# Kernel optimization log

Measured on AMD Instinct MI355X. Metric: run time of the kernel, lower is better.

The kernel has to match this reference:

```python
import jax, jax.numpy as jnp
import numpy as np

TEMPERATURE = 0.07
BASE_TEMPERATURE = 0.07


def setup_inputs() -> dict:
    key = jax.random.key(0)
    k1, k2 = jax.random.split(key)
    features = jax.random.normal(k1, (4096, 2, 128), dtype=jnp.float32)
    labels = jax.random.randint(k2, (4096,), 0, 100, dtype=jnp.int64)
    return {"features": features, "labels": labels}


def reference(features, labels):
    # features: [B, n_views, D], labels: [B]
    B, n_views, D = features.shape
    N = B * n_views

    # label equality mask [B, B]
    lab = labels.reshape(-1, 1)
    mask = (lab == lab.T).astype(jnp.float32)

    # flatten views (C-order, same as torch .view) and L2-normalize
    feat = features.reshape(N, D)
    feat = feat / jnp.clip(jnp.linalg.norm(feat, axis=1, keepdims=True), 1e-12)

    # similarity logits [N, N]
    logits = jnp.matmul(feat, feat.T) / TEMPERATURE
    logits_max = jax.lax.stop_gradient(jnp.max(logits, axis=1, keepdims=True))
    logits = logits - logits_max

    # tile mask to [N, N] (torch .repeat ordering) and remove self-contrast
    mask = jnp.tile(mask, (n_views, n_views))
    logits_mask = 1.0 - jnp.eye(N, dtype=jnp.float32)
    mask = mask * logits_mask

    exp_logits = jnp.exp(logits) * logits_mask
    log_prob = logits - jnp.log(jnp.sum(exp_logits, axis=1, keepdims=True) + 1e-12)

    mask_pos_pairs = jnp.clip(jnp.sum(mask, axis=1), 1.0)
    mean_log_prob_pos = jnp.sum(mask * log_prob, axis=1) / mask_pos_pairs

    loss = -(TEMPERATURE / BASE_TEMPERATURE) * mean_log_prob_pos
    return jnp.mean(loss.reshape(n_views, B))
```

## Files before the change

### kernel.cpp

```cpp
#include <hip/hip_runtime.h>
#include <hip/hip_bf16.h>
#include <hip/hip_fp8.h>
#include <math.h>

#define NB 4096
#define NN 8192
#define DD 128
#define NCLS 100
#define NSPLIT 16
#define CHUNK 64
#define NCHUNK 8

constexpr float INV_T = 14.285714285714286f;
constexpr float EC1   = 20.609929155556620f;
constexpr float EC0   = -20.609929155556620f;
constexpr float LN2   = 0.6931471805599453f;

typedef unsigned char u8;
typedef __attribute__((ext_vector_type(8))) int   v8i;
typedef __attribute__((ext_vector_type(4))) int   v4i;
typedef __attribute__((ext_vector_type(4))) float f32x4;

__global__ __launch_bounds__(256) void k_norm(const float* __restrict__ feat,
                                              u8* __restrict__ fb8,
                                              float* __restrict__ selfdot,
                                              float* __restrict__ out) {
    const int gid = blockIdx.x * 256 + threadIdx.x;
    if (gid == 0) out[0] = 0.0f;
    const int r    = gid >> 6;
    const int lane = threadIdx.x & 63;
    const float2 v = ((const float2*)(feat + (size_t)r * DD))[lane];
    float ss = v.x * v.x + v.y * v.y;
#pragma unroll
    for (int off = 1; off < 64; off <<= 1) ss += __shfl_xor(ss, off, 64);
    const float scale = 1.0f / fmaxf(sqrtf(ss), 1e-12f);
    const __hip_fp8_e4m3 qx(v.x * scale), qy(v.y * scale);
    const unsigned short pack = (unsigned short)qx.__x |
                                ((unsigned short)qy.__x << 8);
    ((unsigned short*)(fb8 + (size_t)r * DD))[lane] = pack;
    const float xb = (float)qx, yb = (float)qy;
    float s2 = xb * xb + yb * yb;
#pragma unroll
    for (int off = 1; off < 64; off <<= 1) s2 += __shfl_xor(s2, off, 64);
    if (lane == 0) selfdot[r] = s2;
}

__device__ __forceinline__ void stage_chunk(const u8* __restrict__ fb8, u8* sbuf,
                                            int jb, int w, int n15, int q) {
#pragma unroll
    for (int h = 0; h < 2; ++h) {
        const int p = w * 2 + h;
        const u8* g = fb8 + (size_t)(jb + (p >> 1) * 16 + n15) * DD + q * 32 + (p & 1) * 16;
        __builtin_amdgcn_global_load_lds(
            (const __attribute__((address_space(1))) void*)g,
            (__attribute__((address_space(3))) void*)(sbuf + p * 1024),
            16, 0, 0);
    }
}

__global__ __launch_bounds__(256, 4) void k_main(const u8* __restrict__ fb8,
                                                 const int* __restrict__ labels,
                                                 float* __restrict__ g_se,
                                                 float* __restrict__ g_ps) {
    __shared__ u8 sB[2][CHUNK * DD];
    __shared__ int slab[512];

    const int tid  = threadIdx.x;
    const int lane = tid & 63;
    const int w    = tid >> 6;
    const int rb   = blockIdx.x >> 4;
    const int js   = blockIdx.x & (NSPLIT - 1);
    const int i0   = rb * 128 + w * 32;
    const int jb0  = js * 512;
    const int q    = lane >> 4;
    const int n15  = lane & 15;

    slab[tid]       = labels[(jb0 + tid) & (NB - 1)];
    slab[tid + 256] = labels[(jb0 + tid + 256) & (NB - 1)];

    v8i af[2];
#pragma unroll
    for (int tt = 0; tt < 2; ++tt) {
        const u8* rp = fb8 + (size_t)(i0 + tt * 16 + n15) * DD + q * 32;
        const v4i lo = *(const v4i*)rp;
        const v4i hi = *(const v4i*)(rp + 16);
        v8i a;
#pragma unroll
        for (int k = 0; k < 4; ++k) { a[k] = lo[k]; a[4 + k] = hi[k]; }
        af[tt] = a;
    }
    int labi[8];
#pragma unroll
    for (int tt = 0; tt < 2; ++tt)
#pragma unroll
        for (int r = 0; r < 4; ++r)
            labi[tt * 4 + r] = labels[(i0 + tt * 16 + q * 4 + r) & (NB - 1)];

    float a_se[8] = {}, a_ps[8] = {};

    stage_chunk(fb8, &sB[0][0], jb0, w, n15, q);
    __syncthreads();

    for (int c = 0; c < NCHUNK; ++c) {
        if (c + 1 < NCHUNK)
            stage_chunk(fb8, &sB[(c + 1) & 1][0], jb0 + (c + 1) * CHUNK, w, n15, q);
        const u8* sb = &sB[c & 1][0];
        const int crel = c * CHUNK;
#pragma unroll
        for (int jt = 0; jt < 4; ++jt) {
            const v4i lo = *(const v4i*)(sb + (jt * 2 + 0) * 1024 + lane * 16);
            const v4i hi = *(const v4i*)(sb + (jt * 2 + 1) * 1024 + lane * 16);
            v8i bb;
#pragma unroll
            for (int k = 0; k < 4; ++k) { bb[k] = lo[k]; bb[4 + k] = hi[k]; }
            const int labj = slab[crel + jt * 16 + n15];
            f32x4 a0 = {0.f, 0.f, 0.f, 0.f}, a1 = {0.f, 0.f, 0.f, 0.f};
            a0 = __builtin_amdgcn_mfma_scale_f32_16x16x128_f8f6f4(
                     af[0], bb, a0, 0, 0, 0, 0x7F7F7F7F, 0, 0x7F7F7F7F);
            a1 = __builtin_amdgcn_mfma_scale_f32_16x16x128_f8f6f4(
                     af[1], bb, a1, 0, 0, 0, 0x7F7F7F7F, 0, 0x7F7F7F7F);
#pragma unroll
            for (int r = 0; r < 4; ++r) {
                const float d0 = a0[r], d1 = a1[r];
                a_se[r]     += __builtin_amdgcn_exp2f(fmaf(d0, EC1, EC0));
                a_se[4 + r] += __builtin_amdgcn_exp2f(fmaf(d1, EC1, EC0));
                a_ps[r]     += (labi[r]     == labj) ? d0 : 0.0f;
                a_ps[4 + r] += (labi[4 + r] == labj) ? d1 : 0.0f;
            }
        }
        __syncthreads();
    }

#pragma unroll
    for (int s = 0; s < 8; ++s) {
        float v1 = a_se[s], v2 = a_ps[s];
#pragma unroll
        for (int off = 1; off < 16; off <<= 1) {
            v1 += __shfl_xor(v1, off, 64);
            v2 += __shfl_xor(v2, off, 64);
        }
        if (n15 == 0) {
            const int row = i0 + (s >> 2) * 16 + q * 4 + (s & 3);
            g_se[js * NN + row] = v1;
            g_ps[js * NN + row] = v2;
        }
    }
}

__global__ __launch_bounds__(256) void k_final(const int* __restrict__ labels,
                                               const float* __restrict__ g_se,
                                               const float* __restrict__ g_ps,
                                               const float* __restrict__ selfdot,
                                               float* __restrict__ out) {
    __shared__ int hist[NCLS];
    const int tid = threadIdx.x;
    for (int i = tid; i < NCLS; i += 256) hist[i] = 0;
    __syncthreads();
    for (int b = tid; b < NB; b += 256) atomicAdd(&hist[labels[b]], 1);
    __syncthreads();

    const int r = blockIdx.x * 256 + tid;
    const int c = labels[r & (NB - 1)];
    float se = 0.f, ps = 0.f;
#pragma unroll
    for (int t = 0; t < NSPLIT; ++t) {
        se += g_se[t * NN + r];
        ps += g_ps[t * NN + r];
    }
    const float sd = selfdot[r];
    se -= __builtin_amdgcn_exp2f(fmaf(sd, EC1, EC0));
    const float ct = (float)(2 * hist[c] - 1);
    const float possum = INV_T * ((ps - sd) - ct);
    const float lg  = __builtin_amdgcn_logf(se + 1e-12f) * LN2;
    const float mlpp = (possum - ct * lg) / fmaxf(ct, 1.0f);
    float v = -mlpp * (1.0f / (float)NN);
#pragma unroll
    for (int off = 1; off < 64; off <<= 1) v += __shfl_xor(v, off, 64);
    __shared__ float sred[4];
    if ((tid & 63) == 0) sred[tid >> 6] = v;
    __syncthreads();
    if (tid == 0) atomicAdd(out, sred[0] + sred[1] + sred[2] + sred[3]);
}

extern "C" void kernel_launch(void* const* d_in, const int* in_sizes, int n_in,
                              void* d_out, int out_size, void* d_ws, size_t ws_size,
                              hipStream_t stream) {
    const float* feat = (const float*)d_in[0];
    const int* labels = (const int*)d_in[1];
    float* out        = (float*)d_out;
    char* ws          = (char*)d_ws;

    u8* fb8         = (u8*)ws;
    float* g_se     = (float*)(ws + (size_t)1 * 1024 * 1024);
    float* g_ps     = g_se + NSPLIT * NN;
    float* selfdot  = g_ps + NSPLIT * NN;

    k_norm<<<NN / 4, 256, 0, stream>>>(feat, fb8, selfdot, out);
    k_main<<<(NN / 128) * NSPLIT, 256, 0, stream>>>(fb8, labels, g_se, g_ps);
    k_final<<<NN / 256, 256, 0, stream>>>(labels, g_se, g_ps, selfdot, out);
}
```

Baseline: 83.54 us.

## Pre-swizzle fp8 features into MFMA fragment layout and load B directly from global

The normalization kernel now writes fp8 features in a 16-row-group layout that matches the MFMA operand fragment, so each lane reads contiguous 16-byte pieces. The main kernel drops the LDS double-buffered staging and its per-chunk barriers, and instead loads B fragments straight from global memory (L2/L1) in a 4x-unrolled loop. This removes LDS traffic and synchronization but relies on cache hits and on the compiler to hide global load latency without explicit prefetching.

```diff
diff --git a/kernel.cpp b/kernel.cpp
--- a/kernel.cpp
+++ b/kernel.cpp
@@ -8,8 +8,6 @@
 #define DD 128
 #define NCLS 100
 #define NSPLIT 16
-#define CHUNK 64
-#define NCHUNK 8
 
 constexpr float INV_T = 14.285714285714286f;
 constexpr float EC1   = 20.609929155556620f;
@@ -20,6 +18,7 @@
 typedef __attribute__((ext_vector_type(8))) int   v8i;
 typedef __attribute__((ext_vector_type(4))) int   v4i;
 typedef __attribute__((ext_vector_type(4))) float f32x4;
+
 
 __global__ __launch_bounds__(256) void k_norm(const float* __restrict__ feat,
                                               u8* __restrict__ fb8,
@@ -37,7 +36,13 @@
     const __hip_fp8_e4m3 qx(v.x * scale), qy(v.y * scale);
     const unsigned short pack = (unsigned short)qx.__x |
                                 ((unsigned short)qy.__x << 8);
-    ((unsigned short*)(fb8 + (size_t)r * DD))[lane] = pack;
+    const int g    = r >> 4;
+    const int n15r = r & 15;
+    const int qc   = lane >> 4;
+    const int hc   = (lane >> 3) & 1;
+    const int bofs = (2 * lane) & 15;
+    *(unsigned short*)(fb8 + (size_t)g * 2048 + hc * 1024 +
+                       ((qc * 16 + n15r) << 4) + bofs) = pack;
     const float xb = (float)qx, yb = (float)qy;
     float s2 = xb * xb + yb * yb;
 #pragma unroll
@@ -45,24 +50,10 @@
     if (lane == 0) selfdot[r] = s2;
 }
 
-__device__ __forceinline__ void stage_chunk(const u8* __restrict__ fb8, u8* sbuf,
-                                            int jb, int w, int n15, int q) {
-#pragma unroll
-    for (int h = 0; h < 2; ++h) {
-        const int p = w * 2 + h;
-        const u8* g = fb8 + (size_t)(jb + (p >> 1) * 16 + n15) * DD + q * 32 + (p & 1) * 16;
-        __builtin_amdgcn_global_load_lds(
-            (const __attribute__((address_space(1))) void*)g,
-            (__attribute__((address_space(3))) void*)(sbuf + p * 1024),
-            16, 0, 0);
-    }
-}
-
 __global__ __launch_bounds__(256, 4) void k_main(const u8* __restrict__ fb8,
                                                  const int* __restrict__ labels,
                                                  float* __restrict__ g_se,
                                                  float* __restrict__ g_ps) {
-    __shared__ u8 sB[2][CHUNK * DD];
     __shared__ int slab[512];
 
     const int tid  = threadIdx.x;
@@ -81,9 +72,9 @@
     v8i af[2];
 #pragma unroll
     for (int tt = 0; tt < 2; ++tt) {
-        const u8* rp = fb8 + (size_t)(i0 + tt * 16 + n15) * DD + q * 32;
-        const v4i lo = *(const v4i*)rp;
-        const v4i hi = *(const v4i*)(rp + 16);
+        const u8* ap = fb8 + (size_t)((i0 >> 4) + tt) * 2048 + lane * 16;
+        const v4i lo = *(const v4i*)ap;
+        const v4i hi = *(const v4i*)(ap + 1024);
         v8i a;
 #pragma unroll
         for (int k = 0; k < 4; ++k) { a[k] = lo[k]; a[4 + k] = hi[k]; }
@@ -98,37 +89,31 @@
 
     float a_se[8] = {}, a_ps[8] = {};
 
-    stage_chunk(fb8, &sB[0][0], jb0, w, n15, q);
     __syncthreads();
 
-    for (int c = 0; c < NCHUNK; ++c) {
-        if (c + 1 < NCHUNK)
-            stage_chunk(fb8, &sB[(c + 1) & 1][0], jb0 + (c + 1) * CHUNK, w, n15, q);
-        const u8* sb = &sB[c & 1][0];
-        const int crel = c * CHUNK;
+    const u8* bbase = fb8 + (size_t)(jb0 >> 4) * 2048 + lane * 16;
+#pragma unroll 4
+    for (int jt = 0; jt < 32; ++jt) {
+        const u8* bp = bbase + (size_t)jt * 2048;
+        const v4i lo = *(const v4i*)bp;
+        const v4i hi = *(const v4i*)(bp + 1024);
+        v8i bb;
 #pragma unroll
-        for (int jt = 0; jt < 4; ++jt) {
-            const v4i lo = *(const v4i*)(sb + (jt * 2 + 0) * 1024 + lane * 16);
-            const v4i hi = *(const v4i*)(sb + (jt * 2 + 1) * 1024 + lane * 16);
-            v8i bb;
+        for (int k = 0; k < 4; ++k) { bb[k] = lo[k]; bb[4 + k] = hi[k]; }
+        const int labj = slab[jt * 16 + n15];
+        f32x4 a0 = {0.f, 0.f, 0.f, 0.f}, a1 = {0.f, 0.f, 0.f, 0.f};
+        a0 = __builtin_amdgcn_mfma_scale_f32_16x16x128_f8f6f4(
+                 af[0], bb, a0, 0, 0, 0, 0x7F7F7F7F, 0, 0x7F7F7F7F);
+        a1 = __builtin_amdgcn_mfma_scale_f32_16x16x128_f8f6f4(
+                 af[1], bb, a1, 0, 0, 0, 0x7F7F7F7F, 0, 0x7F7F7F7F);
 #pragma unroll
-            for (int k = 0; k < 4; ++k) { bb[k] = lo[k]; bb[4 + k] = hi[k]; }
-            const int labj = slab[crel + jt * 16 + n15];
-            f32x4 a0 = {0.f, 0.f, 0.f, 0.f}, a1 = {0.f, 0.f, 0.f, 0.f};
-            a0 = __builtin_amdgcn_mfma_scale_f32_16x16x128_f8f6f4(
-                     af[0], bb, a0, 0, 0, 0, 0x7F7F7F7F, 0, 0x7F7F7F7F);
-            a1 = __builtin_amdgcn_mfma_scale_f32_16x16x128_f8f6f4(
-                     af[1], bb, a1, 0, 0, 0, 0x7F7F7F7F, 0, 0x7F7F7F7F);
-#pragma unroll
-            for (int r = 0; r < 4; ++r) {
-                const float d0 = a0[r], d1 = a1[r];
-                a_se[r]     += __builtin_amdgcn_exp2f(fmaf(d0, EC1, EC0));
-                a_se[4 + r] += __builtin_amdgcn_exp2f(fmaf(d1, EC1, EC0));
-                a_ps[r]     += (labi[r]     == labj) ? d0 : 0.0f;
-                a_ps[4 + r] += (labi[4 + r] == labj) ? d1 : 0.0f;
-            }
+        for (int r = 0; r < 4; ++r) {
+            const float d0 = a0[r], d1 = a1[r];
+            a_se[r]     += __builtin_amdgcn_exp2f(fmaf(d0, EC1, EC0));
+            a_se[4 + r] += __builtin_amdgcn_exp2f(fmaf(d1, EC1, EC0));
+            a_ps[r]     += (labi[r]     == labj) ? d0 : 0.0f;
+            a_ps[4 + r] += (labi[4 + r] == labj) ? d1 : 0.0f;
         }
-        __syncthreads();
     }
 
 #pragma unroll
```

Result: faster. 80.84 us (-3.2%).
